# Optimization experiments

Hardware: AMD Instinct MI355X
Metric: run time of the kernel (lower is better)

Reference implementation:

```python
import jax, jax.numpy as jnp
import numpy as np

B, S_ENC, S_DEC = 8, 128, 256
E, H = 256, 512
VE = VD = 32000


def _run_layer(x, h0, Wi, bi, Wh, bh):
    # Unidirectional Elman layer: h_t = tanh(i2h(x_t) + h2h(h_{t-1})).
    # i2h is time-independent, so precompute for all steps. x: [B,S,in]
    xi = jnp.einsum('bsi,hi->bsh', x, Wi) + bi
    def step(h, xt):
        h = jnp.tanh(xt + h @ Wh.T + bh)
        return h, h
    hT, ys = jax.lax.scan(step, h0, jnp.swapaxes(xi, 0, 1))
    return jnp.swapaxes(ys, 0, 1), hT  # [B,S,H], [B,H]


def _forward(enc_input, target, floats):
    (enc_emb, enc_Wi1, enc_bi1, enc_Wh1, enc_bh1, enc_Wi2, enc_bi2, enc_Wh2, enc_bh2,
     dec_emb, attn_We, attn_be, attn_Wh, attn_bh, attn_V, attn_bV,
     dec_Wi1, dec_bi1, dec_Wh1, dec_bh1, dec_Wi2, dec_bi2, dec_Wh2, dec_bh2,
     out_W, out_b) = floats
    b = enc_input.shape[0]
    # ---- encoder: 2-layer unidirectional Elman RNN over embedded tokens ----
    x = enc_emb[enc_input]                              # [B,S_enc,E]
    h0 = jnp.zeros((b, H), x.dtype)
    out1, h1 = _run_layer(x, h0, enc_Wi1, enc_bi1, enc_Wh1, enc_bh1)
    # RNNBlock passes layer1's final hidden as layer2's initial hidden
    enc_out, hidden = _run_layer(out1, h1, enc_Wi2, enc_bi2, enc_Wh2, enc_bh2)

    # ---- decoder with Bahdanau attention, teacher forcing always on ----
    # dec input at t=0 is target[:,0]; thereafter target[:,t-1]
    dec_tokens = jnp.concatenate([target[:, :1], target[:, :-1]], axis=1)
    dec_x = dec_emb[dec_tokens]                         # [B,S_dec,E]
    # W_enc_out(enc_output) is constant across decode steps -> precompute
    pre_enc = jnp.einsum('bsh,gh->bsg', enc_out, attn_We) + attn_be  # [B,S_enc,H]

    def dec_step(hidden, emb_t):
        align = jnp.tanh(pre_enc + (hidden @ attn_Wh.T + attn_bh)[:, None, :])
        dots = jnp.einsum('bsh,h->bs', align, attn_V[0]) + attn_bV[0]  # [B,S_enc]
        attn = jax.nn.softmax(dots, axis=-1)
        ctx = jnp.einsum('bs,bsh->bh', attn, enc_out)   # [B,H]
        x_t = jnp.concatenate([emb_t, ctx], axis=-1)    # [B,E+H]
        # decoder RNNBlock with seq_len=1: both layers start from `hidden`
        # chain per RNNBlock semantics (layer2 initial hidden = layer1 final)
        h1 = jnp.tanh(x_t @ dec_Wi1.T + dec_bi1 + hidden @ dec_Wh1.T + dec_bh1)
        h2 = jnp.tanh(h1 @ dec_Wi2.T + dec_bi2 + h1 @ dec_Wh2.T + dec_bh2)
        pred = h2 @ out_W.T + out_b                     # [B,VD]
        return h2, pred

    _, preds = jax.lax.scan(dec_step, hidden, jnp.swapaxes(dec_x, 0, 1))
    return jnp.swapaxes(preds, 0, 1)                    # [B,S_dec,VD]


def setup_inputs() -> dict:
    key = jax.random.key(0)
    it = iter(jax.random.split(key, 40))
    def nrm(shape, s=0.05):
        return (jax.random.normal(next(it), shape) * s).astype(jnp.float32)
    return dict(
        enc_input=jax.random.randint(next(it), (B, S_ENC), 0, VE),
        target=jax.random.randint(next(it), (B, S_DEC), 0, VD),
        enc_emb=nrm((VE, E)),
        enc_Wi1=nrm((H, E)), enc_bi1=nrm((H,)), enc_Wh1=nrm((H, H)), enc_bh1=nrm((H,)),
        enc_Wi2=nrm((H, H)), enc_bi2=nrm((H,)), enc_Wh2=nrm((H, H)), enc_bh2=nrm((H,)),
        dec_emb=nrm((VD, E)),
        attn_We=nrm((H, H)), attn_be=nrm((H,)), attn_Wh=nrm((H, H)), attn_bh=nrm((H,)),
        attn_V=nrm((1, H)), attn_bV=nrm((1,)),
        dec_Wi1=nrm((H, E + H)), dec_bi1=nrm((H,)), dec_Wh1=nrm((H, H)), dec_bh1=nrm((H,)),
        dec_Wi2=nrm((H, H)), dec_bi2=nrm((H,)), dec_Wh2=nrm((H, H)), dec_bh2=nrm((H,)),
        out_W=nrm((VD, H)), out_b=nrm((VD,)),
    )


def reference(enc_input, target, enc_emb, enc_Wi1, enc_bi1, enc_Wh1, enc_bh1,
              enc_Wi2, enc_bi2, enc_Wh2, enc_bh2, dec_emb,
              attn_We, attn_be, attn_Wh, attn_bh, attn_V, attn_bV,
              dec_Wi1, dec_bi1, dec_Wh1, dec_bh1, dec_Wi2, dec_bi2, dec_Wh2, dec_bh2,
              out_W, out_b):
    floats = (enc_emb, enc_Wi1, enc_bi1, enc_Wh1, enc_bh1, enc_Wi2, enc_bi2, enc_Wh2, enc_bh2,
              dec_emb, attn_We, attn_be, attn_Wh, attn_bh, attn_V, attn_bV,
              dec_Wi1, dec_bi1, dec_Wh1, dec_bh1, dec_Wi2, dec_bi2, dec_Wh2, dec_bh2,
              out_W, out_b)
    return _forward(enc_input, target, floats)
```

## Files before the change

kernel.cpp:

```cpp
#include <hip/hip_runtime.h>

#define TPB 256
#define NWG 32
#define B_  8
#define H_  512
#define E_  256
#define SE_ 128
#define SD_ 256

typedef unsigned short u16;
typedef unsigned int   u32;
typedef __attribute__((ext_vector_type(4))) float f32x4;
typedef __attribute__((ext_vector_type(8))) short short8;

#define SENTU 0x7FC00001u

__device__ __forceinline__ u16 f2b(float f){
  u32 u = __float_as_uint(f);
  u = (u + 0x7fffu + ((u >> 16) & 1u)) >> 16;
  return (u16)u;
}
__device__ __forceinline__ void b2f2(u32 p, float& a, float& b){
  a = __uint_as_float(p << 16);
  b = __uint_as_float(p & 0xffff0000u);
}
__device__ __forceinline__ float ftanh(float x){
  float e = __expf(2.f * x);
  return 1.f - 2.f / (e + 1.f);
}
__device__ __forceinline__ float red16(float v){
  v += __shfl_xor(v, 1); v += __shfl_xor(v, 2);
  v += __shfl_xor(v, 4); v += __shfl_xor(v, 8);
  return v;
}
__device__ __forceinline__ float sentf(){ return __uint_as_float(SENTU); }
__device__ __forceinline__ bool issent(float x){ return __float_as_uint(x) == SENTU; }

__device__ __forceinline__ float gld(const float* p){
  return __hip_atomic_load(p, __ATOMIC_RELAXED, __HIP_MEMORY_SCOPE_AGENT);
}
__device__ __forceinline__ void gst(float* p, float v){
  __hip_atomic_store(p, v, __ATOMIC_RELAXED, __HIP_MEMORY_SCOPE_AGENT);
}

__device__ __forceinline__ int HPX(int slot,int b,int wg,int r){ return ((slot*8+b)*32+wg)*16+r; }
__device__ __forceinline__ int HPB(int slot,int b){ return (slot*8+b)*512; }
__device__ __forceinline__ int PPX(int slot,int b,int wg,int s){ return ((slot*8+b)*32+wg)*128+s; }
__device__ __forceinline__ int PPB(int slot,int b){ return (slot*8+b)*4096; }

__device__ __forceinline__ void pollgather512(const float* base, float* dst){
  const int tid = threadIdx.x;
  #pragma unroll
  for (int i = 0; i < 2; i++){
    const float* p = base + i*256 + tid;
    float v = gld(p);
    while (!__all(!issent(v))){
      __builtin_amdgcn_s_sleep(1);
      v = gld(p);
    }
    dst[i*256 + tid] = v;
  }
}

struct Inputs {
  const int   *enc_input, *target;
  const float *enc_emb;
  const float *enc_Wi1, *enc_bi1, *enc_Wh1, *enc_bh1;
  const float *enc_Wi2, *enc_bi2, *enc_Wh2, *enc_bh2;
  const float *dec_emb;
  const float *attn_We, *attn_be, *attn_Wh, *attn_bh, *attn_V, *attn_bV;
  const float *dec_Wi1, *dec_bi1, *dec_Wh1, *dec_bh1;
  const float *dec_Wi2, *dec_bi2, *dec_Wh2, *dec_bh2;
  const float *out_W, *out_b;
};
struct Wksp {
  u32*  bar;
  float *hbuf, *h1buf, *h2buf, *partials;
  float *xi1, *xi2, *out1, *encout, *xe;
  u16   *h2all, *wb;
};

constexpr int OFF_A   = 0;
constexpr int OFF_A2  = 17024;
constexpr int OFF_A3  = 34048;
constexpr int OFF_PM  = 50752;
constexpr int OFF_PES = 58944;
constexpr int OFF_STG = 67648;
constexpr int OFF_WRG = 75840;
constexpr int OFF_XV  = 124992;
constexpr int OFF_ES  = 127040;
constexpr int OFF_QS  = 127552;
constexpr int OFF_VS  = 127616;
constexpr int OFF_B1  = 127680;
constexpr int OFF_B2  = 127744;
constexpr int OFF_BH  = 127808;
constexpr int OFF_BSC = 127872;
constexpr int OFF_SCR = 127936;
constexpr int OFF_XV2 = 128000;
constexpr int LDS_BYTES = 130048;

__device__ __forceinline__ void cbar(u32* slots, int wg, u32 target){
  asm volatile("s_waitcnt vmcnt(0)" ::: "memory");
  __syncthreads();
  const int tid = threadIdx.x;
  if (tid < 64){
    if (tid == 0)
      __hip_atomic_store(&slots[wg], target, __ATOMIC_RELAXED, __HIP_MEMORY_SCOPE_AGENT);
    bool done = false;
    do {
      u32 v = __hip_atomic_load(&slots[tid & 31], __ATOMIC_RELAXED, __HIP_MEMORY_SCOPE_AGENT);
      done = (v >= target);
    } while (__ballot(done) != ~0ull);
  }
  __syncthreads();
  asm volatile("" ::: "memory");
}

__device__ void enc_scan(const Wksp& w,
                         const float* __restrict__ Wh, const float* __restrict__ bh,
                         const float* __restrict__ xi, float* __restrict__ outbuf,
                         int b, int wg, u16* WbE, float* xv, float* bscan)
{
  const int tid = threadIdx.x;
  for (int i = tid; i < 16*512; i += TPB){
    int r = i >> 9, j = i & 511;
    WbE[r*522 + j] = f2b(Wh[((size_t)(wg*16 + r))*H_ + j]);
  }
  if (tid < 16) bscan[tid] = bh[wg*16 + tid];
  __syncthreads();
  for (int t = 0; t < SE_; t++){
    pollgather512(&w.hbuf[HPB(t&3, b)], xv);
    __syncthreads();
    int r = tid >> 4, sl = tid & 15;
    float acc = 0.f;
    #pragma unroll
    for (int k = 0; k < 16; k++){
      int j = 2*sl + 32*k;
      u32 pw = *(const u32*)&WbE[r*522 + j];
      float w0, w1; b2f2(pw, w0, w1);
      float2 x = *(const float2*)&xv[j];
      acc += w0*x.x + w1*x.y;
    }
    acc = red16(acc);
    if (sl == 0){
      int row = wg*16 + r;
      float hv = ftanh(xi[((size_t)b*SE_ + t)*H_ + row] + acc + bscan[r]);
      gst(&w.hbuf[HPX((t+1)&3, b, wg, r)], hv);
      gst(&outbuf[((size_t)b*SE_ + t)*H_ + row], hv);
      gst(&w.hbuf[HPX((t+3)&3, b, wg, r)], sentf());
    }
    asm volatile("s_waitcnt vmcnt(0)" ::: "memory");
    __syncthreads();
  }
}

__global__ __launch_bounds__(TPB, 1) void seq2seq_persist(Inputs in, Wksp w)
{
  __shared__ __attribute__((aligned(16))) unsigned char S[LDS_BYTES];
  u16* Wh1s = (u16*)(S + OFF_A);
  u16* Ws2s = (u16*)(S + OFF_A2);
  u16* Wats = (u16*)(S + OFF_A3);
  u16* WaE  = (u16*)(S + OFF_A);
  u16* WbE  = (u16*)(S + OFF_A2);
  float* stgE = (float*)(S + OFF_A3);
  float* Pm   = (float*)(S + OFF_PM);
  float* pes  = (float*)(S + OFF_PES);
  float* STG  = (float*)(S + OFF_STG);
  float* WRG  = (float*)(S + OFF_WRG);
  float* xv   = (float*)(S + OFF_XV);
  float* es   = (float*)(S + OFF_ES);
  float* qs   = (float*)(S + OFF_QS);
  float* Vs   = (float*)(S + OFF_VS);
  float* b1s  = (float*)(S + OFF_B1);
  float* b2s  = (float*)(S + OFF_B2);
  float* bhs  = (float*)(S + OFF_BH);
  float* bscan= (float*)(S + OFF_BSC);
  float* scr  = (float*)(S + OFF_SCR);
  float* xv2  = (float*)(S + OFF_XV2);

  const int bid = blockIdx.x;
  const int c = bid & 7, wg = bid >> 3;
  const int b = c;
  const int tid = threadIdx.x;
  u32* slots = w.bar + c*32;
  u32 bt = 0;

  if (tid < 16){
    gst(&w.hbuf[HPX(0, b, wg, tid)], 0.f);
    #pragma unroll
    for (int s2 = 1; s2 < 4; s2++) gst(&w.hbuf[HPX(s2, b, wg, tid)], sentf());
    #pragma unroll
    for (int s2 = 0; s2 < 4; s2++) gst(&w.h1buf[HPX(s2, b, wg, tid)], sentf());
    #pragma unroll
    for (int s2 = 0; s2 < 3; s2++) gst(&w.h2buf[HPX(s2, b, wg, tid)], sentf());
  }
  if (tid < 128){
    #pragma unroll
    for (int s2 = 0; s2 < 3; s2++) gst(&w.partials[PPX(s2, b, wg, tid)], sentf());
  }

  for (int i = tid; i < 16*256; i += TPB){
    int r = i >> 8, j = i & 255;
    WaE[r*264 + j] = f2b(in.enc_Wi1[((size_t)(wg*16 + r))*E_ + j]);
  }
  if (tid < 16) bscan[tid] = in.enc_bi1[wg*16 + tid];
  __syncthreads();
  for (int k0 = 0; k0 < 8; k0++){
    for (int it = 0; it < 16; it++){
      int tok = in.enc_input[b*SE_ + k0*16 + it];
      stgE[it*256 + tid] = in.enc_emb[(size_t)tok*E_ + tid];
    }
    __syncthreads();
    int r = tid & 15, tt = tid >> 4;
    float acc = 0.f;
    #pragma unroll 16
    for (int j = 0; j < 256; j += 2){
      u32 p = *(const u32*)&WaE[r*264 + j];
      float w0, w1; b2f2(p, w0, w1);
      float2 x = *(const float2*)&stgE[tt*256 + j];
      acc += w0*x.x + w1*x.y;
    }
    w.xi1[((size_t)b*SE_ + k0*16 + tt)*H_ + wg*16 + r] = acc + bscan[r];
    __syncthreads();
  }
  cbar(slots, wg, ++bt);

  enc_scan(w, in.enc_Wh1, in.enc_bh1, w.xi1, w.out1, b, wg, WbE, xv, bscan);
  cbar(slots, wg, ++bt);

  for (int i = tid; i < 16*512; i += TPB){
    int r = i >> 9, j = i & 511;
    WaE[r*522 + j] = f2b(in.enc_Wi2[((size_t)(wg*16 + r))*H_ + j]);
  }
  if (tid < 16){
    bscan[tid] = in.enc_bi2[wg*16 + tid];
    #pragma unroll
    for (int s2 = 1; s2 < 4; s2++) gst(&w.hbuf[HPX(s2, b, wg, tid)], sentf());
  }
  __syncthreads();
  {
    u16* stg2 = (u16*)stgE;
    for (int k0 = 0; k0 < 8; k0++){
      for (int it = 0; it < 16; it++){
        size_t base = ((size_t)b*SE_ + k0*16 + it)*H_;
        stg2[it*512 + tid]       = f2b(gld(&w.out1[base + tid]));
        stg2[it*512 + tid + 256] = f2b(gld(&w.out1[base + tid + 256]));
      }
      __syncthreads();
      int r = tid & 15, tt = tid >> 4;
      float acc = 0.f;
      #pragma unroll 16
      for (int j = 0; j < 512; j += 2){
        u32 p  = *(const u32*)&WaE[r*522 + j];
        u32 s2 = *(const u32*)&stg2[tt*512 + j];
        float w0, w1, s0, s1; b2f2(p, w0, w1); b2f2(s2, s0, s1);
        acc += w0*s0 + w1*s1;
      }
      w.xi2[((size_t)b*SE_ + k0*16 + tt)*H_ + wg*16 + r] = acc + bscan[r];
      __syncthreads();
    }
  }
  cbar(slots, wg, ++bt);

  enc_scan(w, in.enc_Wh2, in.enc_bh2, w.xi2, w.encout, b, wg, WbE, xv, bscan);
  cbar(slots, wg, ++bt);

  for (int i = tid; i < 16*768; i += TPB)
    WRG[i] = in.dec_Wi1[(size_t)(wg*16 + i/768)*768 + (i - (i/768)*768)];
  for (int tb = 0; tb < 32; tb++){
    __syncthreads();
    for (int i = tid; i < 8*256; i += TPB){
      int tt = tb*8 + (i >> 8);
      int tok = in.target[b*SD_ + (tt == 0 ? 0 : tt - 1)];
      STG[i] = in.dec_emb[(size_t)tok*E_ + (i & 255)];
    }
    __syncthreads();
    int r = tid >> 4, sl = tid & 15;
    for (int t2 = 0; t2 < 8; t2++){
      float acc = 0.f;
      #pragma unroll
      for (int k = 0; k < 8; k++){
        int j = 2*sl + 32*k;
        float2 wv = *(const float2*)&WRG[r*768 + j];
        float2 xx = *(const float2*)&STG[t2*256 + j];
        acc += wv.x*xx.x + wv.y*xx.y;
      }
      acc = red16(acc);
      if (sl == 0) w.xe[((size_t)b*SD_ + tb*8 + t2)*H_ + wg*16 + r] = acc;
    }
  }
  for (int sb = 0; sb < 32; sb++){
    __syncthreads();
    for (int i = tid; i < 4*512; i += TPB)
      STG[i] = gld(&w.encout[((size_t)b*SE_ + sb*4 + (i >> 9))*H_ + (i & 511)]);
    __syncthreads();
    int r = tid >> 4, sl = tid & 15;
    const float* wer = in.attn_We + (size_t)(wg*16 + r)*H_;
    float a0=0.f, a1=0.f, a2=0.f, a3=0.f;
    float p0=0.f, p1=0.f, p2=0.f, p3=0.f;
    #pragma unroll
    for (int k = 0; k < 16; k++){
      int j = 2*sl + 32*k;
      float2 wv = *(const float2*)&wer[j];
      float2 x0 = *(const float2*)&STG[j];
      float2 x1 = *(const float2*)&STG[512 + j];
      float2 x2 = *(const float2*)&STG[1024 + j];
      float2 x3 = *(const float2*)&STG[1536 + j];
      a0 += wv.x*x0.x + wv.y*x0.y;  a1 += wv.x*x1.x + wv.y*x1.y;
      a2 += wv.x*x2.x + wv.y*x2.y;  a3 += wv.x*x3.x + wv.y*x3.y;
      float2 cv = *(const float2*)&WRG[r*768 + 256 + j];
      p0 += cv.x*x0.x + cv.y*x0.y;  p1 += cv.x*x1.x + cv.y*x1.y;
      p2 += cv.x*x2.x + cv.y*x2.y;  p3 += cv.x*x3.x + cv.y*x3.y;
    }
    a0 = red16(a0); a1 = red16(a1); a2 = red16(a2); a3 = red16(a3);
    p0 = red16(p0); p1 = red16(p1); p2 = red16(p2); p3 = red16(p3);
    if (sl == 0){
      float bed = in.attn_be[wg*16 + r];
      pes[(sb*4 + 0)*17 + r] = a0 + bed;
      pes[(sb*4 + 1)*17 + r] = a1 + bed;
      pes[(sb*4 + 2)*17 + r] = a2 + bed;
      pes[(sb*4 + 3)*17 + r] = a3 + bed;
      Pm[r*128 + sb*4 + 0] = p0;  Pm[r*128 + sb*4 + 1] = p1;
      Pm[r*128 + sb*4 + 2] = p2;  Pm[r*128 + sb*4 + 3] = p3;
    }
  }
  __syncthreads();
  for (int i = tid; i < 16*512; i += TPB){
    int r = i >> 9, j = i & 511;
    size_t o = ((size_t)(wg*16 + r))*H_ + j;
    Wh1s[r*522 + j] = f2b(in.dec_Wh1[o]);
    Ws2s[r*522 + j] = f2b(in.dec_Wi2[o] + in.dec_Wh2[o]);
    Wats[r*522 + j] = f2b(in.attn_Wh[o]);
  }
  if (tid < 16){
    int row = wg*16 + tid;
    b1s[tid] = in.dec_bi1[row] + in.dec_bh1[row];
    b2s[tid] = in.dec_bi2[row] + in.dec_bh2[row];
    bhs[tid] = in.attn_bh[row];
    Vs[tid]  = in.attn_V[row];
    float hv = gld(&w.hbuf[HPX(0, b, wg, tid)]);
    gst(&w.h2buf[HPX(3, b, wg, tid)], hv);
  }
  if (tid == 0) scr[8] = in.attn_bV[0];
  cbar(slots, wg, ++bt);
  const float bVv = scr[8];

  {
    pollgather512(&w.h2buf[HPB(3, b)], xv);
    __syncthreads();
    int r = tid >> 4, sl = tid & 15;
    float acc = 0.f;
    #pragma unroll
    for (int k = 0; k < 16; k++){
      int j = 2*sl + 32*k;
      u32 p = *(const u32*)&Wats[r*522 + j];
      float w0, w1; b2f2(p, w0, w1);
      float2 x = *(const float2*)&xv[j];
      acc += w0*x.x + w1*x.y;
    }
    acc = red16(acc);
    if (sl == 0) qs[r] = acc + bhs[r];
    __syncthreads();
    if (tid < 128){
      float part = 0.f;
      #pragma unroll
      for (int di = 0; di < 16; di++)
        part += Vs[di] * ftanh(pes[tid*17 + di] + qs[di]);
      gst(&w.partials[PPX(3, b, wg, tid)], part);
    }
  }
  cbar(slots, wg, ++bt);

  for (int t = 0; t < SD_; t++){
    const int sA = (t+3)&3;
    const int sB = t&3;
    const int sP = (t+1)&3;
    pollgather512(&w.h2buf[HPB(sA, b)], xv2);
    __syncthreads();
    {
      int r = tid >> 4, sl = tid & 15;
      float acc = 0.f;
      #pragma unroll
      for (int k = 0; k < 16; k++){
        int j = 2*sl + 32*k;
        u32 p = *(const u32*)&Wats[r*522 + j];
        float w0, w1; b2f2(p, w0, w1);
        float2 x = *(const float2*)&xv2[j];
        acc += w0*x.x + w1*x.y;
      }
      acc = red16(acc);
      if (sl == 0) qs[r] = acc + bhs[r];
    }
    __syncthreads();
    if (tid < 128){
      float part = 0.f;
      #pragma unroll
      for (int di = 0; di < 16; di++)
        part += Vs[di] * ftanh(pes[tid*17 + di] + qs[di]);
      gst(&w.partials[PPX(sA, b, wg, tid)], part);
      const float* pb = &w.partials[PPB(sA, b)];
      float sum;
      for (;;){
        bool ok = true; sum = bVv;
        #pragma unroll
        for (int k = 0; k < 32; k++){
          float x = gld(pb + k*128 + tid);
          ok = ok && !issent(x);
          sum += x;
        }
        if (__all(ok)) break;
        __builtin_amdgcn_s_sleep(1);
      }
      float e = __expf(sum);
      es[tid] = e;
      float d = e;
      d += __shfl_xor(d, 1);  d += __shfl_xor(d, 2);  d += __shfl_xor(d, 4);
      d += __shfl_xor(d, 8);  d += __shfl_xor(d, 16); d += __shfl_xor(d, 32);
      if ((tid & 63) == 0) scr[tid >> 6] = d;
    }
    __syncthreads();
    {
      float rden = 1.f / (scr[0] + scr[1]);
      int r = tid >> 4, sl = tid & 15;
      float acc = 0.f, accP = 0.f;
      #pragma unroll
      for (int k = 0; k < 16; k++){
        int j = 2*sl + 32*k;
        u32 p = *(const u32*)&Wh1s[r*522 + j];
        float w0, w1; b2f2(p, w0, w1);
        float2 x = *(const float2*)&xv2[j];
        acc += w0*x.x + w1*x.y;
      }
      #pragma unroll
      for (int k = 0; k < 8; k++){
        int s = sl + 16*k;
        accP += Pm[r*128 + s] * es[s];
      }
      float tot = red16(acc + accP*rden);
      if (sl == 0){
        int row = wg*16 + r;
        float h1v = ftanh(tot + w.xe[((size_t)b*SD_ + t)*H_ + row] + b1s[r]);
        gst(&w.h1buf[HPX(sB, b, wg, r)], h1v);
        gst(&w.h2buf[HPX(sP, b, wg, r)], sentf());
      }
      if (tid < 128)
        gst(&w.partials[PPX(sP, b, wg, tid)], sentf());
    }
    pollgather512(&w.h1buf[HPB(sB, b)], xv);
    __syncthreads();
    {
      int r = tid >> 4, sl = tid & 15;
      float acc = 0.f;
      #pragma unroll
      for (int k = 0; k < 16; k++){
        int j = 2*sl + 32*k;
        u32 p = *(const u32*)&Ws2s[r*522 + j];
        float w0, w1; b2f2(p, w0, w1);
        float2 x = *(const float2*)&xv[j];
        acc += w0*x.x + w1*x.y;
      }
      acc = red16(acc);
      if (sl == 0){
        float h2v = ftanh(acc + b2s[r]);
        int row = wg*16 + r;
        gst(&w.h2buf[HPX(sB, b, wg, r)], h2v);
        w.h2all[((size_t)(b*SD_ + t))*H_ + row] = f2b(h2v);
        gst(&w.h1buf[HPX((t+2)&3, b, wg, r)], sentf());
      }
    }
    asm volatile("s_waitcnt vmcnt(0)" ::: "memory");
    __syncthreads();
  }
}

__global__ void cvt_bf16(const float* __restrict__ src, u16* __restrict__ dst, int n4){
  int idx = blockIdx.x*blockDim.x + threadIdx.x;
  int stride = gridDim.x*blockDim.x;
  for (int i = idx; i < n4; i += stride){
    float4 v = ((const float4*)src)[i];
    ushort4 o;
    o.x = f2b(v.x); o.y = f2b(v.y); o.z = f2b(v.z); o.w = f2b(v.w);
    ((ushort4*)dst)[i] = o;
  }
}

__global__ __launch_bounds__(256, 1) void out_gemm(const u16* __restrict__ A,
    const u16* __restrict__ Bw, const float* __restrict__ bias, float* __restrict__ out)
{
  __shared__ u16 Al[128*32];
  __shared__ u16 Bl[128*32];
  int tid = threadIdx.x;
  int bidm = blockIdx.x & 15, bidn = blockIdx.x >> 4;
  int m0 = bidm*128, n0 = bidn*128;
  int wv = tid >> 6, l = tid & 63;
  int wm = wv >> 1, wn = wv & 1;
  f32x4 acc[4][4] = {};
  for (int k0 = 0; k0 < 512; k0 += 32){
    __syncthreads();
    #pragma unroll
    for (int rd = 0; rd < 2; rd++){
      int ci = rd*256 + wv*64 + l;
      int row = ci >> 2, qq = ci & 3;
      const u16* ga = A  + (size_t)(m0 + row)*512 + k0 + qq*8;
      const u16* gb = Bw + (size_t)(n0 + row)*512 + k0 + qq*8;
      __builtin_amdgcn_global_load_lds((const __attribute__((address_space(1))) unsigned int*)ga,
          (__attribute__((address_space(3))) unsigned int*)(Al + (rd*256 + wv*64)*8), 16, 0, 0);
      __builtin_amdgcn_global_load_lds((const __attribute__((address_space(1))) unsigned int*)gb,
          (__attribute__((address_space(3))) unsigned int*)(Bl + (rd*256 + wv*64)*8), 16, 0, 0);
    }
    __syncthreads();
    short8 af[4], bf[4];
    int lr = l & 15, lk = l >> 4;
    #pragma unroll
    for (int mi = 0; mi < 4; mi++)
      af[mi] = *(const short8*)(Al + (size_t)(wm*64 + mi*16 + lr)*32 + lk*8);
    #pragma unroll
    for (int ni = 0; ni < 4; ni++)
      bf[ni] = *(const short8*)(Bl + (size_t)(wn*64 + ni*16 + lr)*32 + lk*8);
    #pragma unroll
    for (int mi = 0; mi < 4; mi++)
      #pragma unroll
      for (int ni = 0; ni < 4; ni++)
        acc[mi][ni] = __builtin_amdgcn_mfma_f32_16x16x32_bf16(af[mi], bf[ni], acc[mi][ni], 0, 0, 0);
  }
  #pragma unroll
  for (int ni = 0; ni < 4; ni++){
    int col = n0 + wn*64 + ni*16 + (l & 15);
    float bb = bias[col];
    #pragma unroll
    for (int mi = 0; mi < 4; mi++){
      int row = m0 + wm*64 + mi*16 + (l >> 4)*4;
      #pragma unroll
      for (int r = 0; r < 4; r++)
        out[(size_t)(row + r)*32000 + col] = acc[mi][ni][r] + bb;
    }
  }
}

extern "C" void kernel_launch(void* const* d_in, const int* in_sizes, int n_in,
                              void* d_out, int out_size, void* d_ws, size_t ws_size,
                              hipStream_t stream)
{
  (void)in_sizes; (void)n_in; (void)out_size; (void)ws_size;
  Inputs in;
  in.enc_input = (const int*)d_in[0];
  in.target    = (const int*)d_in[1];
  in.enc_emb   = (const float*)d_in[2];
  in.enc_Wi1   = (const float*)d_in[3];  in.enc_bi1 = (const float*)d_in[4];
  in.enc_Wh1   = (const float*)d_in[5];  in.enc_bh1 = (const float*)d_in[6];
  in.enc_Wi2   = (const float*)d_in[7];  in.enc_bi2 = (const float*)d_in[8];
  in.enc_Wh2   = (const float*)d_in[9];  in.enc_bh2 = (const float*)d_in[10];
  in.dec_emb   = (const float*)d_in[11];
  in.attn_We   = (const float*)d_in[12]; in.attn_be = (const float*)d_in[13];
  in.attn_Wh   = (const float*)d_in[14]; in.attn_bh = (const float*)d_in[15];
  in.attn_V    = (const float*)d_in[16]; in.attn_bV = (const float*)d_in[17];
  in.dec_Wi1   = (const float*)d_in[18]; in.dec_bi1 = (const float*)d_in[19];
  in.dec_Wh1   = (const float*)d_in[20]; in.dec_bh1 = (const float*)d_in[21];
  in.dec_Wi2   = (const float*)d_in[22]; in.dec_bi2 = (const float*)d_in[23];
  in.dec_Wh2   = (const float*)d_in[24]; in.dec_bh2 = (const float*)d_in[25];
  in.out_W     = (const float*)d_in[26]; in.out_b   = (const float*)d_in[27];

  char* ws = (char*)d_ws;
  char* od = (char*)d_out;
  Wksp w;
  w.bar      = (u32*)ws;
  w.hbuf     = (float*)(ws + 1024);
  w.h1buf    = (float*)(ws + 66560);
  w.h2buf    = (float*)(ws + 132096);
  w.partials = (float*)(ws + 197632);
  w.h2all    = (u16*)  (ws + 721920);
  w.wb       = (u16*)  (ws + 2819072);
  w.xi1    = (float*)(od);
  w.xi2    = (float*)(od + (1 << 21));
  w.out1   = (float*)(od + 2*(1 << 21));
  w.encout = (float*)(od + 3*(1 << 21));
  w.xe     = (float*)(od + 4*(1 << 21));

  hipMemsetAsync(d_ws, 0, 1024, stream);
  cvt_bf16<<<dim3(4096), dim3(256), 0, stream>>>(in.out_W, w.wb, 32000*512/4);
  seq2seq_persist<<<dim3(256), dim3(TPB), 0, stream>>>(in, w);
  out_gemm<<<dim3(4000), dim3(256), 0, stream>>>(w.h2all, w.wb, in.out_b, (float*)d_out);
}
```

Baseline: 2.787 ms.

## Switch recurrent matvecs to fp16 dot2 and vectorize hidden-state polling

Recurrent weight slices in LDS are now stored as fp16 instead of bf16, and the gathered hidden vectors are converted to packed half2 so each inner step uses a single fdot2 instruction rather than unpacking and two FMAs. The poll-gather now uses 128 threads with dwordx4 loads carrying cache-bypass bits instead of two scalar atomic loads per thread. The decoder's Wh1 matvec is hoisted to run before the partial-sum poll so it overlaps with waiting for other workgroups. This trades bf16 range for fp16 precision on weights and activations, and it changes the LDS row padding.

```diff
diff --git a/kernel.cpp b/kernel.cpp
--- a/kernel.cpp
+++ b/kernel.cpp
@@ -7,11 +7,13 @@
 #define E_  256
 #define SE_ 128
 #define SD_ 256
+#define WS  530
 
 typedef unsigned short u16;
 typedef unsigned int   u32;
 typedef __attribute__((ext_vector_type(4))) float f32x4;
 typedef __attribute__((ext_vector_type(8))) short short8;
+typedef __attribute__((ext_vector_type(2))) _Float16 half2v;
 
 #define SENTU 0x7FC00001u
 
@@ -20,6 +22,10 @@
   u = (u + 0x7fffu + ((u >> 16) & 1u)) >> 16;
   return (u16)u;
 }
+__device__ __forceinline__ u16 f2h(float f){
+  _Float16 h = (_Float16)f;
+  return __builtin_bit_cast(unsigned short, h);
+}
 __device__ __forceinline__ void b2f2(u32 p, float& a, float& b){
   a = __uint_as_float(p << 16);
   b = __uint_as_float(p & 0xffff0000u);
@@ -35,6 +41,13 @@
 }
 __device__ __forceinline__ float sentf(){ return __uint_as_float(SENTU); }
 __device__ __forceinline__ bool issent(float x){ return __float_as_uint(x) == SENTU; }
+__device__ __forceinline__ float dot2h(half2v w, half2v x, float acc){
+#if __has_builtin(__builtin_amdgcn_fdot2)
+  return __builtin_amdgcn_fdot2(w, x, acc, false);
+#else
+  return acc + (float)w.x * (float)x.x + (float)w.y * (float)x.y;
+#endif
+}
 
 __device__ __forceinline__ float gld(const float* p){
   return __hip_atomic_load(p, __ATOMIC_RELAXED, __HIP_MEMORY_SCOPE_AGENT);
@@ -48,17 +61,23 @@
 __device__ __forceinline__ int PPX(int slot,int b,int wg,int s){ return ((slot*8+b)*32+wg)*128+s; }
 __device__ __forceinline__ int PPB(int slot,int b){ return (slot*8+b)*4096; }
 
-__device__ __forceinline__ void pollgather512(const float* base, float* dst){
+__device__ __forceinline__ void pollgather_h(const float* base, half2v* dsth){
   const int tid = threadIdx.x;
-  #pragma unroll
-  for (int i = 0; i < 2; i++){
-    const float* p = base + i*256 + tid;
-    float v = gld(p);
-    while (!__all(!issent(v))){
+  if (tid < 128){
+    const float* p = base + tid*4;
+    f32x4 v;
+    for (;;){
+      asm volatile("global_load_dwordx4 %0, %1, off sc0 sc1\n\ts_waitcnt vmcnt(0)"
+                   : "=v"(v) : "v"(p) : "memory");
+      bool ok = !issent(v.x) && !issent(v.y) && !issent(v.z) && !issent(v.w);
+      if (__all(ok)) break;
       __builtin_amdgcn_s_sleep(1);
-      v = gld(p);
-    }
-    dst[i*256 + tid] = v;
+    }
+    half2v h0, h1;
+    h0.x = (_Float16)v.x; h0.y = (_Float16)v.y;
+    h1.x = (_Float16)v.z; h1.y = (_Float16)v.w;
+    dsth[tid*2]     = h0;
+    dsth[tid*2 + 1] = h1;
   }
 }
 
@@ -83,21 +102,21 @@
 constexpr int OFF_A   = 0;
 constexpr int OFF_A2  = 17024;
 constexpr int OFF_A3  = 34048;
-constexpr int OFF_PM  = 50752;
-constexpr int OFF_PES = 58944;
-constexpr int OFF_STG = 67648;
-constexpr int OFF_WRG = 75840;
-constexpr int OFF_XV  = 124992;
-constexpr int OFF_ES  = 127040;
-constexpr int OFF_QS  = 127552;
-constexpr int OFF_VS  = 127616;
-constexpr int OFF_B1  = 127680;
-constexpr int OFF_B2  = 127744;
-constexpr int OFF_BH  = 127808;
-constexpr int OFF_BSC = 127872;
-constexpr int OFF_SCR = 127936;
-constexpr int OFF_XV2 = 128000;
-constexpr int LDS_BYTES = 130048;
+constexpr int OFF_PM  = 51008;
+constexpr int OFF_PES = 59200;
+constexpr int OFF_STG = 67904;
+constexpr int OFF_WRG = 76096;
+constexpr int OFF_XVH = 125248;
+constexpr int OFF_XV2H= 126272;
+constexpr int OFF_ES  = 127296;
+constexpr int OFF_QS  = 127808;
+constexpr int OFF_VS  = 127872;
+constexpr int OFF_B1  = 127936;
+constexpr int OFF_B2  = 128000;
+constexpr int OFF_BH  = 128064;
+constexpr int OFF_BSC = 128128;
+constexpr int OFF_SCR = 128192;
+constexpr int LDS_BYTES = 128256;
 
 __device__ __forceinline__ void cbar(u32* slots, int wg, u32 target){
   asm volatile("s_waitcnt vmcnt(0)" ::: "memory");
@@ -119,27 +138,24 @@
 __device__ void enc_scan(const Wksp& w,
                          const float* __restrict__ Wh, const float* __restrict__ bh,
                          const float* __restrict__ xi, float* __restrict__ outbuf,
-                         int b, int wg, u16* WbE, float* xv, float* bscan)
+                         int b, int wg, u16* WbE, half2v* xvh, float* bscan)
 {
   const int tid = threadIdx.x;
   for (int i = tid; i < 16*512; i += TPB){
     int r = i >> 9, j = i & 511;
-    WbE[r*522 + j] = f2b(Wh[((size_t)(wg*16 + r))*H_ + j]);
+    WbE[r*WS + j] = f2h(Wh[((size_t)(wg*16 + r))*H_ + j]);
   }
   if (tid < 16) bscan[tid] = bh[wg*16 + tid];
   __syncthreads();
   for (int t = 0; t < SE_; t++){
-    pollgather512(&w.hbuf[HPB(t&3, b)], xv);
+    pollgather_h(&w.hbuf[HPB(t&3, b)], xvh);
     __syncthreads();
     int r = tid >> 4, sl = tid & 15;
     float acc = 0.f;
     #pragma unroll
     for (int k = 0; k < 16; k++){
-      int j = 2*sl + 32*k;
-      u32 pw = *(const u32*)&WbE[r*522 + j];
-      float w0, w1; b2f2(pw, w0, w1);
-      float2 x = *(const float2*)&xv[j];
-      acc += w0*x.x + w1*x.y;
+      int jj = sl + 16*k;
+      acc = dot2h(*(const half2v*)&WbE[r*WS + 2*jj], xvh[jj], acc);
     }
     acc = red16(acc);
     if (sl == 0){
@@ -167,7 +183,8 @@
   float* pes  = (float*)(S + OFF_PES);
   float* STG  = (float*)(S + OFF_STG);
   float* WRG  = (float*)(S + OFF_WRG);
-  float* xv   = (float*)(S + OFF_XV);
+  half2v* xvh  = (half2v*)(S + OFF_XVH);
+  half2v* xv2h = (half2v*)(S + OFF_XV2H);
   float* es   = (float*)(S + OFF_ES);
   float* qs   = (float*)(S + OFF_QS);
   float* Vs   = (float*)(S + OFF_VS);
@@ -176,7 +193,6 @@
   float* bhs  = (float*)(S + OFF_BH);
   float* bscan= (float*)(S + OFF_BSC);
   float* scr  = (float*)(S + OFF_SCR);
-  float* xv2  = (float*)(S + OFF_XV2);
 
   const int bid = blockIdx.x;
   const int c = bid & 7, wg = bid >> 3;
@@ -225,7 +241,7 @@
   }
   cbar(slots, wg, ++bt);
 
-  enc_scan(w, in.enc_Wh1, in.enc_bh1, w.xi1, w.out1, b, wg, WbE, xv, bscan);
+  enc_scan(w, in.enc_Wh1, in.enc_bh1, w.xi1, w.out1, b, wg, WbE, xvh, bscan);
   cbar(slots, wg, ++bt);
 
   for (int i = tid; i < 16*512; i += TPB){
@@ -262,7 +278,7 @@
   }
   cbar(slots, wg, ++bt);
 
-  enc_scan(w, in.enc_Wh2, in.enc_bh2, w.xi2, w.encout, b, wg, WbE, xv, bscan);
+  enc_scan(w, in.enc_Wh2, in.enc_bh2, w.xi2, w.encout, b, wg, WbE, xvh, bscan);
   cbar(slots, wg, ++bt);
 
   for (int i = tid; i < 16*768; i += TPB)
@@ -328,9 +344,9 @@
   for (int i = tid; i < 16*512; i += TPB){
     int r = i >> 9, j = i & 511;
     size_t o = ((size_t)(wg*16 + r))*H_ + j;
-    Wh1s[r*522 + j] = f2b(in.dec_Wh1[o]);
-    Ws2s[r*522 + j] = f2b(in.dec_Wi2[o] + in.dec_Wh2[o]);
-    Wats[r*522 + j] = f2b(in.attn_Wh[o]);
+    Wh1s[r*WS + j] = f2h(in.dec_Wh1[o]);
+    Ws2s[r*WS + j] = f2h(in.dec_Wi2[o] + in.dec_Wh2[o]);
+    Wats[r*WS + j] = f2h(in.attn_Wh[o]);
   }
   if (tid < 16){
     int row = wg*16 + tid;
@@ -346,17 +362,14 @@
   const float bVv = scr[8];
 
   {
-    pollgather512(&w.h2buf[HPB(3, b)], xv);
+    pollgather_h(&w.h2buf[HPB(3, b)], xv2h);
     __syncthreads();
     int r = tid >> 4, sl = tid & 15;
     float acc = 0.f;
     #pragma unroll
     for (int k = 0; k < 16; k++){
-      int j = 2*sl + 32*k;
-      u32 p = *(const u32*)&Wats[r*522 + j];
-      float w0, w1; b2f2(p, w0, w1);
-      float2 x = *(const float2*)&xv[j];
-      acc += w0*x.x + w1*x.y;
+      int jj = sl + 16*k;
+      acc = dot2h(*(const half2v*)&Wats[r*WS + 2*jj], xv2h[jj], acc);
     }
     acc = red16(acc);
     if (sl == 0) qs[r] = acc + bhs[r];
@@ -371,25 +384,22 @@
   }
   cbar(slots, wg, ++bt);
 
+  const int r = tid >> 4, sl = tid & 15;
   for (int t = 0; t < SD_; t++){
     const int sA = (t+3)&3;
     const int sB = t&3;
     const int sP = (t+1)&3;
-    pollgather512(&w.h2buf[HPB(sA, b)], xv2);
+    pollgather_h(&w.h2buf[HPB(sA, b)], xv2h);
     __syncthreads();
     {
-      int r = tid >> 4, sl = tid & 15;
-      float acc = 0.f;
+      float aq = 0.f;
       #pragma unroll
       for (int k = 0; k < 16; k++){
-        int j = 2*sl + 32*k;
-        u32 p = *(const u32*)&Wats[r*522 + j];
-        float w0, w1; b2f2(p, w0, w1);
-        float2 x = *(const float2*)&xv2[j];
-        acc += w0*x.x + w1*x.y;
-      }
-      acc = red16(acc);
-      if (sl == 0) qs[r] = acc + bhs[r];
+        int jj = sl + 16*k;
+        aq = dot2h(*(const half2v*)&Wats[r*WS + 2*jj], xv2h[jj], aq);
+      }
+      aq = red16(aq);
+      if (sl == 0) qs[r] = aq + bhs[r];
     }
     __syncthreads();
     if (tid < 128){
@@ -398,6 +408,14 @@
       for (int di = 0; di < 16; di++)
         part += Vs[di] * ftanh(pes[tid*17 + di] + qs[di]);
       gst(&w.partials[PPX(sA, b, wg, tid)], part);
+    }
+    float ah = 0.f;
+    #pragma unroll
+    for (int k = 0; k < 16; k++){
+      int jj = sl + 16*k;
+      ah = dot2h(*(const half2v*)&Wh1s[r*WS + 2*jj], xv2h[jj], ah);
+    }
+    if (tid < 128){
       const float* pb = &w.partials[PPB(sA, b)];
       float sum;
       for (;;){
@@ -421,22 +439,13 @@
     __syncthreads();
     {
       float rden = 1.f / (scr[0] + scr[1]);
-      int r = tid >> 4, sl = tid & 15;
-      float acc = 0.f, accP = 0.f;
-      #pragma unroll
-      for (int k = 0; k < 16; k++){
-        int j = 2*sl + 32*k;
-        u32 p = *(const u32*)&Wh1s[r*522 + j];
-        float w0, w1; b2f2(p, w0, w1);
-        float2 x = *(const float2*)&xv2[j];
-        acc += w0*x.x + w1*x.y;
-      }
+      float accP = 0.f;
       #pragma unroll
       for (int k = 0; k < 8; k++){
         int s = sl + 16*k;
         accP += Pm[r*128 + s] * es[s];
       }
-      float tot = red16(acc + accP*rden);
+      float tot = red16(ah + accP*rden);
       if (sl == 0){
         int row = wg*16 + r;
         float h1v = ftanh(tot + w.xe[((size_t)b*SD_ + t)*H_ + row] + b1s[r]);
@@ -446,18 +455,14 @@
       if (tid < 128)
         gst(&w.partials[PPX(sP, b, wg, tid)], sentf());
     }
-    pollgather512(&w.h1buf[HPB(sB, b)], xv);
+    pollgather_h(&w.h1buf[HPB(sB, b)], xvh);
     __syncthreads();
     {
-      int r = tid >> 4, sl = tid & 15;
       float acc = 0.f;
       #pragma unroll
       for (int k = 0; k < 16; k++){
-        int j = 2*sl + 32*k;
-        u32 p = *(const u32*)&Ws2s[r*522 + j];
-        float w0, w1; b2f2(p, w0, w1);
-        float2 x = *(const float2*)&xv[j];
-        acc += w0*x.x + w1*x.y;
+        int jj = sl + 16*k;
+        acc = dot2h(*(const half2v*)&Ws2s[r*WS + 2*jj], xvh[jj], acc);
       }
       acc = red16(acc);
       if (sl == 0){
```

After: 2.492 ms (median of 2 runs). -10.6%, faster.
